# Kernel tuning notes

Hardware: AMD Instinct MI355X
Metric: run time of the kernel (lower is better)

## Reference

```python
import jax, jax.numpy as jnp
import numpy as np

N_NODES = 50000
N_EDGES = 600000
D = 128


def setup_inputs() -> dict:
    key = jax.random.key(0)
    ks = jax.random.split(key, 8)
    s = 0.05
    return {
        "x": jax.random.normal(ks[0], (N_NODES, D), jnp.float32),
        "edge_index": jax.random.randint(ks[1], (2, N_EDGES), 0, N_NODES, jnp.int64),
        "edge_attr": jax.random.normal(ks[2], (N_EDGES, D), jnp.float32),
        "We1": jax.random.normal(ks[3], (3 * D, D), jnp.float32) * s,
        "be1": jnp.zeros((D,), jnp.float32),
        "We2": jax.random.normal(ks[4], (D, D), jnp.float32) * s,
        "be2": jnp.zeros((D,), jnp.float32),
        "Wn1": jax.random.normal(ks[5], (2 * D, D), jnp.float32) * s,
        "bn1": jnp.zeros((D,), jnp.float32),
        "Wn2": jax.random.normal(ks[6], (D, D), jnp.float32) * s,
        "bn2": jnp.zeros((D,), jnp.float32),
    }


def reference(x, edge_index, edge_attr, We1, be1, We2, be2, Wn1, bn1, Wn2, bn2):
    src = edge_index[0]
    dest = edge_index[1]
    n = x.shape[0]
    # edge model: MLP on [x_src | x_dest | edge_attr]  -> [E, D]
    e_in = jnp.concatenate([x[src], x[dest], edge_attr], axis=-1)
    e = jax.nn.relu(e_in @ We1 + be1) @ We2 + be2
    # node model: scatter-mean of updated edge_attr into dest nodes
    agg = jax.ops.segment_sum(e, dest, num_segments=n)
    cnt = jax.ops.segment_sum(jnp.ones((e.shape[0],), e.dtype), dest, num_segments=n)
    agg = agg / jnp.maximum(cnt, 1.0)[:, None]
    n_in = jnp.concatenate([x, agg], axis=-1)
    x_out = jax.nn.relu(n_in @ Wn1 + bn1) @ Wn2 + bn2
    return x_out, e
```

## Files before the change

### kernel.cpp

```cpp
#include <hip/hip_runtime.h>
#include <hip/hip_bf16.h>

#define DD 128

typedef short bf16x8 __attribute__((ext_vector_type(8)));
typedef float f32x4 __attribute__((ext_vector_type(4)));
typedef float f32x2v __attribute__((ext_vector_type(2)));

__device__ __forceinline__ unsigned short f2b(float f) {
  unsigned int u = __float_as_uint(f);
  u = u + 0x7FFFu + ((u >> 16) & 1u);
  return (unsigned short)(u >> 16);
}

#define GLDS16(gp, lp) __builtin_amdgcn_global_load_lds( \
    (const __attribute__((address_space(1))) unsigned int*)(const void*)(gp), \
    (__attribute__((address_space(3))) unsigned int*)(void*)(lp), 16, 0, 0)

__global__ __launch_bounds__(256) void cvt_x_kernel(const float* __restrict__ x,
                                                    unsigned short* __restrict__ xb, int n4) {
  const int i = blockIdx.x * 256 + threadIdx.x;
  if (i < n4) {
    const float4 v = reinterpret_cast<const float4*>(x)[i];
    ushort4 o;
    o.x = f2b(v.x); o.y = f2b(v.y); o.z = f2b(v.z); o.w = f2b(v.w);
    reinterpret_cast<ushort4*>(xb)[i] = o;
  }
}

__global__ void count_kernel(const int* __restrict__ ei, int* __restrict__ cnt, int E) {
  int i = blockIdx.x * blockDim.x + threadIdx.x;
  if (i < E) atomicAdd(&cnt[ei[E + i]], 1);
}

__global__ __launch_bounds__(256) void scan_a(const int* __restrict__ cnt,
                                              int* __restrict__ off,
                                              int* __restrict__ bsum, int N) {
  __shared__ int wsum[4];
  const int t = threadIdx.x;
  const int i0 = blockIdx.x * 1024 + t * 4;
  int4 v = {0, 0, 0, 0};
  if (i0 + 3 < N) v = *reinterpret_cast<const int4*>(cnt + i0);
  else {
    if (i0 < N)     v.x = cnt[i0];
    if (i0 + 1 < N) v.y = cnt[i0 + 1];
    if (i0 + 2 < N) v.z = cnt[i0 + 2];
    if (i0 + 3 < N) v.w = cnt[i0 + 3];
  }
  const int s1 = v.x, s2 = s1 + v.y, s3 = s2 + v.z, tot = s3 + v.w;
  const int lane = t & 63, wv = t >> 6;
  int sc = tot;
#pragma unroll
  for (int d = 1; d < 64; d <<= 1) {
    int u = __shfl_up(sc, d);
    if (lane >= d) sc += u;
  }
  if (lane == 63) wsum[wv] = sc;
  __syncthreads();
  int wpre = 0;
  for (int w = 0; w < wv; ++w) wpre += wsum[w];
  const int excl = wpre + sc - tot;
  if (i0 < N)     off[i0]     = excl;
  if (i0 + 1 < N) off[i0 + 1] = excl + s1;
  if (i0 + 2 < N) off[i0 + 2] = excl + s2;
  if (i0 + 3 < N) off[i0 + 3] = excl + s3;
  if (t == 255) bsum[blockIdx.x] = wpre + sc;
}

__global__ void scan_b(int* __restrict__ bsum, int B) {
  const int t = threadIdx.x;
  const int v0 = (t < B) ? bsum[t] : 0;
  int v = v0;
#pragma unroll
  for (int d = 1; d < 64; d <<= 1) {
    int u = __shfl_up(v, d);
    if (t >= d) v += u;
  }
  if (t < B) bsum[t] = v - v0;
}

__global__ __launch_bounds__(256) void scan_c(int* __restrict__ off, int* __restrict__ cur,
                                              const int* __restrict__ bsum, int N, int E) {
  const int t = threadIdx.x;
  const int add = bsum[blockIdx.x];
  const int i0 = blockIdx.x * 1024 + t * 4;
#pragma unroll
  for (int k = 0; k < 4; ++k) {
    const int i = i0 + k;
    if (i < N) {
      const int o = off[i] + add;
      off[i] = o;
      cur[i] = o;
    }
  }
  if (blockIdx.x == 0 && t == 0) off[N] = E;
}

__global__ void fill_kernel(const int* __restrict__ ei, int* __restrict__ cur,
                            int* __restrict__ perm, int E) {
  int i = blockIdx.x * blockDim.x + threadIdx.x;
  if (i < E) {
    const int d = ei[E + i];
    const int pos = atomicAdd(&cur[d], 1);
    perm[pos] = i;
  }
}

__global__ __launch_bounds__(256, 2) void edge_mlp_kernel(
    const unsigned short* __restrict__ xb,
    const int* __restrict__ ei,
    const float* __restrict__ ea,
    const float* __restrict__ We1,
    const float* __restrict__ be1,
    const float* __restrict__ We2,
    const float* __restrict__ be2,
    float* __restrict__ e_out,
    int E)
{
  __shared__ __align__(16) unsigned short xs_lds[64][128];
  __shared__ __align__(16) unsigned short xd_lds[64][128];
  __shared__ __align__(16) unsigned short ea_lds[64][128];
  __shared__ __align__(16) unsigned short h_lds[64][136];
  __shared__ int srcs[64], dsts[64];

  const int tid  = threadIdx.x;
  const int wv   = tid >> 6;
  const int lane = tid & 63;
  const int lg   = lane >> 4;
  const int lm   = lane & 15;

  bf16x8 w1f[12][2];
  bf16x8 w2f[4][2];
  float b1[2], b2[2];
#pragma unroll
  for (int nf = 0; nf < 2; ++nf) {
    const int n = wv * 32 + nf * 16 + lm;
    b1[nf] = be1[n];
    b2[nf] = be2[n];
#pragma unroll
    for (int kb = 0; kb < 12; ++kb) {
      bf16x8 f;
#pragma unroll
      for (int j = 0; j < 8; ++j)
        f[j] = (short)f2b(We1[(kb * 32 + lg * 8 + j) * DD + n]);
      w1f[kb][nf] = f;
    }
#pragma unroll
    for (int kb = 0; kb < 4; ++kb) {
      bf16x8 f;
#pragma unroll
      for (int j = 0; j < 8; ++j)
        f[j] = (short)f2b(We2[(kb * 32 + lg * 8 + j) * DD + n]);
      w2f[kb][nf] = f;
    }
  }

  const int ntiles = E >> 6;
  for (int tile = blockIdx.x; tile < ntiles; tile += gridDim.x) {
    const int ebase = tile << 6;
    __syncthreads();

    if (tid < 64)       srcs[tid]      = ei[ebase + tid];
    else if (tid < 128) dsts[tid - 64] = ei[E + ebase + tid - 64];
    __syncthreads();

    {
#pragma unroll
      for (int wl = 0; wl < 4; ++wl) {
        const int r0 = wv * 16 + wl * 4;
        const int r  = r0 + (lane >> 4);
        const int ch = (lane & 15) ^ (r & 7);
        GLDS16(xb + (size_t)srcs[r] * DD + ch * 8, &xs_lds[r0][0]);
        GLDS16(xb + (size_t)dsts[r] * DD + ch * 8, &xd_lds[r0][0]);
      }
    }

    {
      f32x4 va[4], vb[4];
#pragma unroll
      for (int it = 0; it < 4; ++it) {
        const int q = tid + it * 256;
        const int r = q >> 4;
        const int c = q & 15;
        const float* p = ea + (size_t)(ebase + r) * DD + c * 8;
        va[it] = __builtin_nontemporal_load(reinterpret_cast<const f32x4*>(p));
        vb[it] = __builtin_nontemporal_load(reinterpret_cast<const f32x4*>(p + 4));
      }
#pragma unroll
      for (int it = 0; it < 4; ++it) {
        const int q = tid + it * 256;
        const int r = q >> 4;
        const int c = q & 15;
        bf16x8 o;
        o[0] = (short)f2b(va[it][0]); o[1] = (short)f2b(va[it][1]);
        o[2] = (short)f2b(va[it][2]); o[3] = (short)f2b(va[it][3]);
        o[4] = (short)f2b(vb[it][0]); o[5] = (short)f2b(vb[it][1]);
        o[6] = (short)f2b(vb[it][2]); o[7] = (short)f2b(vb[it][3]);
        *reinterpret_cast<bf16x8*>(&ea_lds[r][(c ^ (r & 7)) * 8]) = o;
      }
    }
    __syncthreads();

    f32x4 acc[4][2];
#pragma unroll
    for (int mf = 0; mf < 4; ++mf)
#pragma unroll
      for (int nf = 0; nf < 2; ++nf)
        acc[mf][nf] = (f32x4){0.f, 0.f, 0.f, 0.f};

#pragma unroll
    for (int kb = 0; kb < 12; ++kb) {
      const unsigned short (*blk)[128] = (kb < 4) ? xs_lds : (kb < 8) ? xd_lds : ea_lds;
      const int kl = kb & 3;
      bf16x8 a[4];
#pragma unroll
      for (int mf = 0; mf < 4; ++mf) {
        const int r = mf * 16 + lm;
        a[mf] = *reinterpret_cast<const bf16x8*>(&blk[r][((kl * 4 + lg) ^ (r & 7)) * 8]);
      }
#pragma unroll
      for (int mf = 0; mf < 4; ++mf)
#pragma unroll
        for (int nf = 0; nf < 2; ++nf)
          acc[mf][nf] = __builtin_amdgcn_mfma_f32_16x16x32_bf16(a[mf], w1f[kb][nf], acc[mf][nf], 0, 0, 0);
    }

#pragma unroll
    for (int mf = 0; mf < 4; ++mf)
#pragma unroll
      for (int nf = 0; nf < 2; ++nf)
#pragma unroll
        for (int rg = 0; rg < 4; ++rg) {
          const int m = mf * 16 + lg * 4 + rg;
          const int n = wv * 32 + nf * 16 + lm;
          float v = acc[mf][nf][rg] + b1[nf];
          h_lds[m][n] = f2b(v > 0.f ? v : 0.f);
        }
    __syncthreads();

    f32x4 acc2[4][2];
#pragma unroll
    for (int mf = 0; mf < 4; ++mf)
#pragma unroll
      for (int nf = 0; nf < 2; ++nf)
        acc2[mf][nf] = (f32x4){0.f, 0.f, 0.f, 0.f};

#pragma unroll
    for (int kb = 0; kb < 4; ++kb) {
      bf16x8 a[4];
#pragma unroll
      for (int mf = 0; mf < 4; ++mf)
        a[mf] = *reinterpret_cast<const bf16x8*>(&h_lds[mf * 16 + lm][kb * 32 + lg * 8]);
#pragma unroll
      for (int mf = 0; mf < 4; ++mf)
#pragma unroll
        for (int nf = 0; nf < 2; ++nf)
          acc2[mf][nf] = __builtin_amdgcn_mfma_f32_16x16x32_bf16(a[mf], w2f[kb][nf], acc2[mf][nf], 0, 0, 0);
    }

#pragma unroll
    for (int mf = 0; mf < 4; ++mf)
#pragma unroll
      for (int rg = 0; rg < 4; ++rg) {
        const int gm = ebase + mf * 16 + lg * 4 + rg;
#pragma unroll
        for (int nf = 0; nf < 2; ++nf) {
          const int n = wv * 32 + nf * 16 + lm;
          __builtin_nontemporal_store(acc2[mf][nf][rg] + b2[nf],
                                      &e_out[(size_t)gm * DD + n]);
        }
      }
  }
}

__global__ __launch_bounds__(256) void agg_kernel(const float* __restrict__ e_out,
                                                  const int* __restrict__ off,
                                                  const int* __restrict__ perm,
                                                  float* __restrict__ agg, int N) {
  const int wv   = threadIdx.x >> 6;
  const int lane = threadIdx.x & 63;
  const int nid  = blockIdx.x * 4 + wv;
  if (nid >= N) return;
  const int o0 = off[nid], o1 = off[nid + 1];
  float sx = 0.f, sy = 0.f;
  int j = o0;
  for (; j + 8 <= o1; j += 8) {
    int r[8];
#pragma unroll
    for (int k = 0; k < 8; ++k) r[k] = perm[j + k];
    f32x2v v[8];
#pragma unroll
    for (int k = 0; k < 8; ++k)
      v[k] = __builtin_nontemporal_load(
          reinterpret_cast<const f32x2v*>(e_out + (size_t)r[k] * DD + (lane << 1)));
#pragma unroll
    for (int k = 0; k < 8; ++k) { sx += v[k][0]; sy += v[k][1]; }
  }
  if (j + 4 <= o1) {
    int r[4];
#pragma unroll
    for (int k = 0; k < 4; ++k) r[k] = perm[j + k];
    f32x2v v[4];
#pragma unroll
    for (int k = 0; k < 4; ++k)
      v[k] = __builtin_nontemporal_load(
          reinterpret_cast<const f32x2v*>(e_out + (size_t)r[k] * DD + (lane << 1)));
#pragma unroll
    for (int k = 0; k < 4; ++k) { sx += v[k][0]; sy += v[k][1]; }
    j += 4;
  }
  for (; j < o1; ++j) {
    const int r = perm[j];
    const f32x2v v = __builtin_nontemporal_load(
        reinterpret_cast<const f32x2v*>(e_out + (size_t)r * DD + (lane << 1)));
    sx += v[0]; sy += v[1];
  }
  const int deg = o1 - o0;
  const float inv = deg > 0 ? 1.f / (float)deg : 0.f;
  float2 o;
  o.x = sx * inv;
  o.y = sy * inv;
  *reinterpret_cast<float2*>(agg + (size_t)nid * DD + (lane << 1)) = o;
}

__global__ __launch_bounds__(256, 2) void node_mlp_kernel(
    const float* __restrict__ x,
    const float* __restrict__ Wn1,
    const float* __restrict__ bn1,
    const float* __restrict__ Wn2,
    const float* __restrict__ bn2,
    float* __restrict__ xout,
    int N)
{
  __shared__ __align__(16) unsigned short A_lds[64][264];
  __shared__ __align__(16) unsigned short h_lds[64][136];

  const int tid  = threadIdx.x;
  const int wv   = tid >> 6;
  const int lane = tid & 63;
  const int lg   = lane >> 4;
  const int lm   = lane & 15;

  bf16x8 w1f[8][2];
  bf16x8 w2f[4][2];
  float b1[2], b2[2];
#pragma unroll
  for (int nf = 0; nf < 2; ++nf) {
    const int n = wv * 32 + nf * 16 + lm;
    b1[nf] = bn1[n];
    b2[nf] = bn2[n];
#pragma unroll
    for (int kb = 0; kb < 8; ++kb) {
      bf16x8 f;
#pragma unroll
      for (int j = 0; j < 8; ++j)
        f[j] = (short)f2b(Wn1[(kb * 32 + lg * 8 + j) * DD + n]);
      w1f[kb][nf] = f;
    }
#pragma unroll
    for (int kb = 0; kb < 4; ++kb) {
      bf16x8 f;
#pragma unroll
      for (int j = 0; j < 8; ++j)
        f[j] = (short)f2b(Wn2[(kb * 32 + lg * 8 + j) * DD + n]);
      w2f[kb][nf] = f;
    }
  }

  const int ntiles = (N + 63) >> 6;
  for (int tile = blockIdx.x; tile < ntiles; tile += gridDim.x) {
    const int nbase = tile << 6;
    __syncthreads();

#pragma unroll
    for (int it = 0; it < 16; ++it) {
      const int q = tid + it * 256;
      const int r = q >> 6;
      const int c = q & 63;
      int gr = nbase + r;
      if (gr >= N) gr = N - 1;
      float4 v;
      if (c < 32) v = *reinterpret_cast<const float4*>(x + (size_t)gr * DD + (c << 2));
      else        v = *reinterpret_cast<const float4*>(xout + (size_t)gr * DD + ((c - 32) << 2));
      unsigned short* dst = &A_lds[r][c << 2];
      dst[0] = f2b(v.x); dst[1] = f2b(v.y); dst[2] = f2b(v.z); dst[3] = f2b(v.w);
    }
    __syncthreads();

    f32x4 acc[4][2];
#pragma unroll
    for (int mf = 0; mf < 4; ++mf)
#pragma unroll
      for (int nf = 0; nf < 2; ++nf)
        acc[mf][nf] = (f32x4){0.f, 0.f, 0.f, 0.f};

#pragma unroll
    for (int kb = 0; kb < 8; ++kb) {
      bf16x8 a[4];
#pragma unroll
      for (int mf = 0; mf < 4; ++mf)
        a[mf] = *reinterpret_cast<const bf16x8*>(&A_lds[mf * 16 + lm][kb * 32 + lg * 8]);
#pragma unroll
      for (int mf = 0; mf < 4; ++mf)
#pragma unroll
        for (int nf = 0; nf < 2; ++nf)
          acc[mf][nf] = __builtin_amdgcn_mfma_f32_16x16x32_bf16(a[mf], w1f[kb][nf], acc[mf][nf], 0, 0, 0);
    }

#pragma unroll
    for (int mf = 0; mf < 4; ++mf)
#pragma unroll
      for (int nf = 0; nf < 2; ++nf)
#pragma unroll
        for (int rg = 0; rg < 4; ++rg) {
          const int m = mf * 16 + lg * 4 + rg;
          const int n = wv * 32 + nf * 16 + lm;
          float v = acc[mf][nf][rg] + b1[nf];
          h_lds[m][n] = f2b(v > 0.f ? v : 0.f);
        }
    __syncthreads();

    f32x4 acc2[4][2];
#pragma unroll
    for (int mf = 0; mf < 4; ++mf)
#pragma unroll
      for (int nf = 0; nf < 2; ++nf)
        acc2[mf][nf] = (f32x4){0.f, 0.f, 0.f, 0.f};

#pragma unroll
    for (int kb = 0; kb < 4; ++kb) {
      bf16x8 a[4];
#pragma unroll
      for (int mf = 0; mf < 4; ++mf)
        a[mf] = *reinterpret_cast<const bf16x8*>(&h_lds[mf * 16 + lm][kb * 32 + lg * 8]);
#pragma unroll
      for (int mf = 0; mf < 4; ++mf)
#pragma unroll
        for (int nf = 0; nf < 2; ++nf)
          acc2[mf][nf] = __builtin_amdgcn_mfma_f32_16x16x32_bf16(a[mf], w2f[kb][nf], acc2[mf][nf], 0, 0, 0);
    }

#pragma unroll
    for (int mf = 0; mf < 4; ++mf)
#pragma unroll
      for (int rg = 0; rg < 4; ++rg) {
        const int gm = nbase + mf * 16 + lg * 4 + rg;
        if (gm < N) {
#pragma unroll
          for (int nf = 0; nf < 2; ++nf) {
            const int n = wv * 32 + nf * 16 + lm;
            xout[(size_t)gm * DD + n] = acc2[mf][nf][rg] + b2[nf];
          }
        }
      }
  }
}

extern "C" void kernel_launch(void* const* d_in, const int* in_sizes, int n_in,
                              void* d_out, int out_size, void* d_ws, size_t ws_size,
                              hipStream_t stream) {
  const float* x   = (const float*)d_in[0];
  const int*   ei  = (const int*)d_in[1];
  const float* ea  = (const float*)d_in[2];
  const float* We1 = (const float*)d_in[3];
  const float* be1 = (const float*)d_in[4];
  const float* We2 = (const float*)d_in[5];
  const float* be2 = (const float*)d_in[6];
  const float* Wn1 = (const float*)d_in[7];
  const float* bn1 = (const float*)d_in[8];
  const float* Wn2 = (const float*)d_in[9];
  const float* bn2 = (const float*)d_in[10];

  const int N = in_sizes[0] / DD;
  const int E = in_sizes[2] / DD;

  float* out   = (float*)d_out;
  float* xout  = out;
  float* e_out = out + (size_t)N * DD;

  unsigned short* xb = (unsigned short*)xout;

  int* cnt  = (int*)d_ws;
  int* off  = cnt + N;
  int* cur  = off + N + 1;
  int* perm = cur + N;
  int* bsum = perm + E;

  const int SCAN_B = (N + 1023) / 1024;

  hipMemsetAsync(cnt, 0, (size_t)N * sizeof(int), stream);

  cvt_x_kernel<<<(N * DD / 4 + 255) / 256, 256, 0, stream>>>(x, xb, N * DD / 4);

  count_kernel<<<(E + 255) / 256, 256, 0, stream>>>(ei, cnt, E);
  scan_a<<<SCAN_B, 256, 0, stream>>>(cnt, off, bsum, N);
  scan_b<<<1, 64, 0, stream>>>(bsum, SCAN_B);
  scan_c<<<SCAN_B, 256, 0, stream>>>(off, cur, bsum, N, E);
  fill_kernel<<<(E + 255) / 256, 256, 0, stream>>>(ei, cur, perm, E);

  edge_mlp_kernel<<<2048, 256, 0, stream>>>(xb, ei, ea, We1, be1, We2, be2, e_out, E);

  agg_kernel<<<(N + 3) / 4, 256, 0, stream>>>(e_out, off, perm, xout, N);

  const int node_tiles = (N + 63) / 64;
  node_mlp_kernel<<<node_tiles, 256, 0, stream>>>(x, Wn1, bn1, Wn2, bn2, xout, N);
}
```

Before: 370.6 us.

## Double-buffer edge MLP tiles with async LDS loads and 32-edge tiles

Restructures the edge MLP kernel into a software pipeline. The gathers of the next tile's x_src, x_dest and edge_attr rows go into a second LDS buffer through global_load_lds while the current tile is computed, and edge indices are prefetched two tiles ahead. The tile shrinks from 64 to 32 edges and edge_attr is now staged as fp32 in LDS and converted to bf16 when fragments are read. Custom barriers with explicit vmcnt waits replace __syncthreads, which adds hazard risk if the wait counts are wrong and gives less MFMA work per barrier.

```diff
diff --git a/kernel.cpp b/kernel.cpp
--- a/kernel.cpp
+++ b/kernel.cpp
@@ -16,6 +16,15 @@
 #define GLDS16(gp, lp) __builtin_amdgcn_global_load_lds( \
     (const __attribute__((address_space(1))) unsigned int*)(const void*)(gp), \
     (__attribute__((address_space(3))) unsigned int*)(void*)(lp), 16, 0, 0)
+
+#define BAR_LGKM() do { \
+    asm volatile("s_waitcnt lgkmcnt(0)" ::: "memory"); \
+    __builtin_amdgcn_sched_barrier(0); \
+    __builtin_amdgcn_s_barrier(); } while (0)
+#define BAR_VM(nn) do { \
+    asm volatile("s_waitcnt vmcnt(" #nn ") lgkmcnt(0)" ::: "memory"); \
+    __builtin_amdgcn_sched_barrier(0); \
+    __builtin_amdgcn_s_barrier(); } while (0)
 
 __global__ __launch_bounds__(256) void cvt_x_kernel(const float* __restrict__ x,
                                                     unsigned short* __restrict__ xb, int n4) {
@@ -117,11 +126,11 @@
     float* __restrict__ e_out,
     int E)
 {
-  __shared__ __align__(16) unsigned short xs_lds[64][128];
-  __shared__ __align__(16) unsigned short xd_lds[64][128];
-  __shared__ __align__(16) unsigned short ea_lds[64][128];
-  __shared__ __align__(16) unsigned short h_lds[64][136];
-  __shared__ int srcs[64], dsts[64];
+  __shared__ __align__(16) unsigned short xs_lds[2][32][128];
+  __shared__ __align__(16) unsigned short xd_lds[2][32][128];
+  __shared__ __align__(16) float          ea_lds[2][32][128];
+  __shared__ __align__(16) unsigned short h_lds[32][136];
+  __shared__ int sidx[2][64];
 
   const int tid  = threadIdx.x;
   const int wv   = tid >> 6;
@@ -155,78 +164,106 @@
     }
   }
 
-  const int ntiles = E >> 6;
-  for (int tile = blockIdx.x; tile < ntiles; tile += gridDim.x) {
-    const int ebase = tile << 6;
-    __syncthreads();
-
-    if (tid < 64)       srcs[tid]      = ei[ebase + tid];
-    else if (tid < 128) dsts[tid - 64] = ei[E + ebase + tid - 64];
-    __syncthreads();
-
-    {
-#pragma unroll
-      for (int wl = 0; wl < 4; ++wl) {
-        const int r0 = wv * 16 + wl * 4;
-        const int r  = r0 + (lane >> 4);
-        const int ch = (lane & 15) ^ (r & 7);
-        GLDS16(xb + (size_t)srcs[r] * DD + ch * 8, &xs_lds[r0][0]);
-        GLDS16(xb + (size_t)dsts[r] * DD + ch * 8, &xd_lds[r0][0]);
+  const int ntiles = E >> 5;
+  const int stride = gridDim.x;
+  const int bid    = blockIdx.x;
+
+  auto ISSUE = [&](int tt, int bi) {
+    const int eb = tt << 5;
+#pragma unroll
+    for (int wl = 0; wl < 2; ++wl) {
+      const int r0 = wv * 8 + wl * 4;
+      const int r  = r0 + (lane >> 4);
+      const int ch = (lane & 15) ^ (r & 7);
+      GLDS16(xb + (size_t)sidx[bi][r] * DD + ch * 8,      &xs_lds[bi][r0][0]);
+      GLDS16(xb + (size_t)sidx[bi][32 + r] * DD + ch * 8, &xd_lds[bi][r0][0]);
+    }
+#pragma unroll
+    for (int wl = 0; wl < 4; ++wl) {
+      const int r0 = wv * 8 + wl * 2;
+      const int r  = r0 + (lane >> 5);
+      const int ch = (lane & 31) ^ (r & 7);
+      GLDS16(ea + (size_t)(eb + r) * DD + ch * 4, &ea_lds[bi][r0][0]);
+    }
+  };
+
+  {
+    const int t0 = bid, t1 = bid + stride;
+    if (tid < 64) {
+      if (t0 < ntiles) {
+        const int eb = t0 << 5;
+        sidx[0][tid] = (tid < 32) ? ei[eb + tid] : ei[E + eb + tid - 32];
       }
-    }
-
-    {
-      f32x4 va[4], vb[4];
-#pragma unroll
-      for (int it = 0; it < 4; ++it) {
-        const int q = tid + it * 256;
-        const int r = q >> 4;
-        const int c = q & 15;
-        const float* p = ea + (size_t)(ebase + r) * DD + c * 8;
-        va[it] = __builtin_nontemporal_load(reinterpret_cast<const f32x4*>(p));
-        vb[it] = __builtin_nontemporal_load(reinterpret_cast<const f32x4*>(p + 4));
+      if (t1 < ntiles) {
+        const int eb = t1 << 5;
+        sidx[1][tid] = (tid < 32) ? ei[eb + tid] : ei[E + eb + tid - 32];
       }
-#pragma unroll
-      for (int it = 0; it < 4; ++it) {
-        const int q = tid + it * 256;
-        const int r = q >> 4;
-        const int c = q & 15;
-        bf16x8 o;
-        o[0] = (short)f2b(va[it][0]); o[1] = (short)f2b(va[it][1]);
-        o[2] = (short)f2b(va[it][2]); o[3] = (short)f2b(va[it][3]);
-        o[4] = (short)f2b(vb[it][0]); o[5] = (short)f2b(vb[it][1]);
-        o[6] = (short)f2b(vb[it][2]); o[7] = (short)f2b(vb[it][3]);
-        *reinterpret_cast<bf16x8*>(&ea_lds[r][(c ^ (r & 7)) * 8]) = o;
-      }
-    }
-    __syncthreads();
-
-    f32x4 acc[4][2];
-#pragma unroll
-    for (int mf = 0; mf < 4; ++mf)
+    }
+  }
+  BAR_LGKM();
+  if (bid < ntiles) ISSUE(bid, 0);
+  BAR_VM(0);
+
+  for (int i = 0; ; ++i) {
+    const int t = bid + i * stride;
+    if (t >= ntiles) break;
+    const int b  = i & 1;
+    const int eb = t << 5;
+    const int tn = t + stride;
+    const int t2 = t + 2 * stride;
+
+    int idxreg = 0;
+    const bool h2 = (t2 < ntiles) && (tid < 64);
+    if (h2) {
+      const int e2 = t2 << 5;
+      idxreg = (tid < 32) ? ei[e2 + tid] : ei[E + e2 + tid - 32];
+    }
+
+    if (tn < ntiles) ISSUE(tn, b ^ 1);
+
+    f32x4 acc[2][2];
+#pragma unroll
+    for (int mf = 0; mf < 2; ++mf)
 #pragma unroll
       for (int nf = 0; nf < 2; ++nf)
         acc[mf][nf] = (f32x4){0.f, 0.f, 0.f, 0.f};
 
 #pragma unroll
     for (int kb = 0; kb < 12; ++kb) {
-      const unsigned short (*blk)[128] = (kb < 4) ? xs_lds : (kb < 8) ? xd_lds : ea_lds;
-      const int kl = kb & 3;
-      bf16x8 a[4];
-#pragma unroll
-      for (int mf = 0; mf < 4; ++mf) {
-        const int r = mf * 16 + lm;
-        a[mf] = *reinterpret_cast<const bf16x8*>(&blk[r][((kl * 4 + lg) ^ (r & 7)) * 8]);
+      bf16x8 a[2];
+      if (kb < 8) {
+        const unsigned short (*blk)[128] = (kb < 4) ? xs_lds[b] : xd_lds[b];
+        const int kl = kb & 3;
+#pragma unroll
+        for (int mf = 0; mf < 2; ++mf) {
+          const int r = mf * 16 + lm;
+          a[mf] = *reinterpret_cast<const bf16x8*>(&blk[r][((kl * 4 + lg) ^ (r & 7)) * 8]);
+        }
+      } else {
+        const int c0 = (kb - 8) * 8 + lg * 2;
+#pragma unroll
+        for (int mf = 0; mf < 2; ++mf) {
+          const int r  = mf * 16 + lm;
+          const int sw = r & 7;
+          const f32x4 lo = *reinterpret_cast<const f32x4*>(&ea_lds[b][r][(c0 ^ sw) * 4]);
+          const f32x4 hi = *reinterpret_cast<const f32x4*>(&ea_lds[b][r][((c0 + 1) ^ sw) * 4]);
+          bf16x8 o;
+          o[0] = (short)f2b(lo[0]); o[1] = (short)f2b(lo[1]);
+          o[2] = (short)f2b(lo[2]); o[3] = (short)f2b(lo[3]);
+          o[4] = (short)f2b(hi[0]); o[5] = (short)f2b(hi[1]);
+          o[6] = (short)f2b(hi[2]); o[7] = (short)f2b(hi[3]);
+          a[mf] = o;
+        }
       }
 #pragma unroll
-      for (int mf = 0; mf < 4; ++mf)
+      for (int mf = 0; mf < 2; ++mf)
 #pragma unroll
         for (int nf = 0; nf < 2; ++nf)
           acc[mf][nf] = __builtin_amdgcn_mfma_f32_16x16x32_bf16(a[mf], w1f[kb][nf], acc[mf][nf], 0, 0, 0);
     }
 
 #pragma unroll
-    for (int mf = 0; mf < 4; ++mf)
+    for (int mf = 0; mf < 2; ++mf)
 #pragma unroll
       for (int nf = 0; nf < 2; ++nf)
 #pragma unroll
@@ -236,33 +273,35 @@
           float v = acc[mf][nf][rg] + b1[nf];
           h_lds[m][n] = f2b(v > 0.f ? v : 0.f);
         }
-    __syncthreads();
-
-    f32x4 acc2[4][2];
-#pragma unroll
-    for (int mf = 0; mf < 4; ++mf)
+    BAR_LGKM();
+
+    if (h2) sidx[b][tid] = idxreg;
+
+    f32x4 acc2[2][2];
+#pragma unroll
+    for (int mf = 0; mf < 2; ++mf)
 #pragma unroll
       for (int nf = 0; nf < 2; ++nf)
         acc2[mf][nf] = (f32x4){0.f, 0.f, 0.f, 0.f};
 
 #pragma unroll
     for (int kb = 0; kb < 4; ++kb) {
-      bf16x8 a[4];
-#pragma unroll
-      for (int mf = 0; mf < 4; ++mf)
+      bf16x8 a[2];
+#pragma unroll
+      for (int mf = 0; mf < 2; ++mf)
         a[mf] = *reinterpret_cast<const bf16x8*>(&h_lds[mf * 16 + lm][kb * 32 + lg * 8]);
 #pragma unroll
-      for (int mf = 0; mf < 4; ++mf)
+      for (int mf = 0; mf < 2; ++mf)
 #pragma unroll
         for (int nf = 0; nf < 2; ++nf)
           acc2[mf][nf] = __builtin_amdgcn_mfma_f32_16x16x32_bf16(a[mf], w2f[kb][nf], acc2[mf][nf], 0, 0, 0);
     }
 
 #pragma unroll
-    for (int mf = 0; mf < 4; ++mf)
+    for (int mf = 0; mf < 2; ++mf)
 #pragma unroll
       for (int rg = 0; rg < 4; ++rg) {
-        const int gm = ebase + mf * 16 + lg * 4 + rg;
+        const int gm = eb + mf * 16 + lg * 4 + rg;
 #pragma unroll
         for (int nf = 0; nf < 2; ++nf) {
           const int n = wv * 32 + nf * 16 + lm;
@@ -270,6 +309,8 @@
                                       &e_out[(size_t)gm * DD + n]);
         }
       }
+
+    BAR_VM(16);
   }
 }
 
```

After: 442.8 us. 1.19x slower.
